# Optimization experiments

Measured on AMD Instinct MI355X. Metric: run time of the kernel, lower is better.

## Reference

```python
import jax, jax.numpy as jnp
import numpy as np

N_HEADS, N_LEVELS, N_POINTS = 8, 4, 4
D_MODEL, D_FFN = 256, 2048
NQ, BS = 900, 4
SPATIAL = np.array([[128, 128], [64, 64], [32, 32], [16, 16]], dtype=np.int64)
HW = int((SPATIAL[:, 0] * SPATIAL[:, 1]).sum())


def _ln(x, g, b):
    mu = x.mean(-1, keepdims=True)
    var = x.var(-1, keepdims=True)
    return (x - mu) / jnp.sqrt(var + 1e-5) * g + b


def _lin(x, w, b):
    return x @ w.T + b


def _msdeform_attn(query, refp, mem, ss, starts, so_w, so_b, aw_w, aw_b, vp_w, vp_b, op_w, op_b):
    # query: (bs, nq, d), refp: (bs, nq, L, 2) in [0,1], mem: (bs, hw, d)
    bs, nq, d = query.shape
    hd = d // N_HEADS
    value = _lin(mem, vp_w, vp_b).reshape(bs, -1, N_HEADS, hd)  # (bs, hw, H, hd)
    offsets = _lin(query, so_w, so_b).reshape(bs, nq, N_HEADS, N_LEVELS, N_POINTS, 2)
    aw = _lin(query, aw_w, aw_b).reshape(bs, nq, N_HEADS, N_LEVELS * N_POINTS)
    aw = jax.nn.softmax(aw, axis=-1).reshape(bs, nq, N_HEADS, N_LEVELS, N_POINTS)
    # offset normalizer is (W, H) per level
    normalizer = jnp.asarray(ss[:, ::-1].copy(), dtype=query.dtype)  # (L, 2)
    loc = refp[:, :, None, :, None, :] + offsets / normalizer[None, None, None, :, None, :]
    out = jnp.zeros((bs, nq, N_HEADS, hd), dtype=query.dtype)
    for l in range(N_LEVELS):
        h_l, w_l = int(ss[l, 0]), int(ss[l, 1])
        vl = value[:, starts[l]:starts[l] + h_l * w_l]  # (bs, h*w, H, hd)
        # grid_sample align_corners=False: pixel coord = loc*size - 0.5
        x = loc[:, :, :, l, :, 0] * w_l - 0.5  # (bs, nq, H, P)
        y = loc[:, :, :, l, :, 1] * h_l - 0.5
        x0 = jnp.floor(x)
        y0 = jnp.floor(y)
        fx = x - x0
        fy = y - y0

        def gather(ix, iy, wgt):
            valid = (ix >= 0) & (ix < w_l) & (iy >= 0) & (iy < h_l)
            idx = (jnp.clip(iy, 0, h_l - 1) * w_l + jnp.clip(ix, 0, w_l - 1)).astype(jnp.int32)
            # (bs, nq, H, P) -> (bs, nq*P, H) to match vl's (bs, hw, H, hd)
            idxt = idx.transpose(0, 1, 3, 2).reshape(bs, nq * N_POINTS, N_HEADS)
            g = jnp.take_along_axis(vl, idxt[..., None], axis=1)  # (bs, nq*P, H, hd)
            g = g.reshape(bs, nq, N_POINTS, N_HEADS, hd).transpose(0, 1, 3, 2, 4)
            return g * (wgt * valid)[..., None]

        x0i = x0.astype(jnp.int32)
        y0i = y0.astype(jnp.int32)
        sampled = (gather(x0i, y0i, (1 - fx) * (1 - fy))
                   + gather(x0i + 1, y0i, fx * (1 - fy))
                   + gather(x0i, y0i + 1, (1 - fx) * fy)
                   + gather(x0i + 1, y0i + 1, fx * fy))  # (bs, nq, H, P, hd)
        out = out + (sampled * aw[:, :, :, l, :, None]).sum(axis=3)
    return _lin(out.reshape(bs, nq, d), op_w, op_b)


def _fwd(tgt, query_pos, memory, ref_points,
         sa_in_w, sa_in_b, sa_out_w, sa_out_b,
         ln1_g, ln1_b, ln2_g, ln2_b, ln3_g, ln3_b,
         so_w, so_b, aw_w, aw_b, vp_w, vp_b, op_w, op_b,
         ff1_w, ff1_b, ff2_w, ff2_b, spatial_shapes, level_start_index):
    nq, bs, d = tgt.shape
    hd = d // N_HEADS
    ss = np.asarray(spatial_shapes)
    starts = np.asarray(level_start_index)
    # ---- self attention (q = k = tgt + pos, v = tgt) ----
    qk = tgt + query_pos
    q = _lin(qk, sa_in_w[:d], sa_in_b[:d]).reshape(nq, bs, N_HEADS, hd)
    k = _lin(qk, sa_in_w[d:2 * d], sa_in_b[d:2 * d]).reshape(nq, bs, N_HEADS, hd)
    v = _lin(tgt, sa_in_w[2 * d:], sa_in_b[2 * d:]).reshape(nq, bs, N_HEADS, hd)
    scores = jnp.einsum('qbhd,kbhd->bhqk', q, k) / np.sqrt(hd).astype(tgt.dtype)
    attn = jax.nn.softmax(scores, axis=-1)
    sa = jnp.einsum('bhqk,kbhd->qbhd', attn, v).reshape(nq, bs, d)
    sa = _lin(sa, sa_out_w, sa_out_b)
    tgt = _ln(tgt + sa, ln2_g, ln2_b)
    # ---- deformable cross attention ----
    ca = _msdeform_attn((tgt + query_pos).transpose(1, 0, 2),
                        ref_points.transpose(1, 0, 2, 3),
                        memory.transpose(1, 0, 2), ss, starts,
                        so_w, so_b, aw_w, aw_b, vp_w, vp_b, op_w, op_b)
    tgt = _ln(tgt + ca.transpose(1, 0, 2), ln1_g, ln1_b)
    # ---- FFN ----
    ff = _lin(jax.nn.relu(_lin(tgt, ff1_w, ff1_b)), ff2_w, ff2_b)
    return _ln(tgt + ff, ln3_g, ln3_b)


def setup_inputs() -> dict:
    key = jax.random.key(0)
    ks = iter(jax.random.split(key, 32))
    d, dffn = D_MODEL, D_FFN
    nofs = N_HEADS * N_LEVELS * N_POINTS
    w = lambda *s: jax.random.normal(next(ks), s, dtype=jnp.float32) * 0.02
    starts = np.concatenate([[0], np.cumsum(SPATIAL[:, 0] * SPATIAL[:, 1])[:-1]]).astype(np.int64)
    return {
        'tgt': jax.random.normal(next(ks), (NQ, BS, d), dtype=jnp.float32),
        'query_pos': jax.random.normal(next(ks), (NQ, BS, d), dtype=jnp.float32),
        'memory': jax.random.normal(next(ks), (HW, BS, d), dtype=jnp.float32),
        'ref_points': jax.random.uniform(next(ks), (NQ, BS, N_LEVELS, 2), dtype=jnp.float32),
        'sa_in_w': w(3 * d, d), 'sa_in_b': w(3 * d), 'sa_out_w': w(d, d), 'sa_out_b': w(d),
        'ln1_g': jnp.ones((d,)), 'ln1_b': jnp.zeros((d,)),
        'ln2_g': jnp.ones((d,)), 'ln2_b': jnp.zeros((d,)),
        'ln3_g': jnp.ones((d,)), 'ln3_b': jnp.zeros((d,)),
        'so_w': w(nofs * 2, d), 'so_b': jax.random.normal(next(ks), (nofs * 2,), dtype=jnp.float32) * 0.5,
        'aw_w': w(nofs, d), 'aw_b': w(nofs),
        'vp_w': w(d, d), 'vp_b': w(d), 'op_w': w(d, d), 'op_b': w(d),
        'ff1_w': w(dffn, d), 'ff1_b': w(dffn), 'ff2_w': w(d, dffn), 'ff2_b': w(d),
        'spatial_shapes': SPATIAL, 'level_start_index': starts,
    }


def reference(tgt, query_pos, memory, ref_points, sa_in_w, sa_in_b, sa_out_w, sa_out_b, ln1_g, ln1_b, ln2_g, ln2_b, ln3_g, ln3_b, so_w, so_b, aw_w, aw_b, vp_w, vp_b, op_w, op_b, ff1_w, ff1_b, ff2_w, ff2_b, spatial_shapes, level_start_index):
    return _fwd(tgt, query_pos, memory, ref_points, sa_in_w, sa_in_b, sa_out_w, sa_out_b,
                ln1_g, ln1_b, ln2_g, ln2_b, ln3_g, ln3_b, so_w, so_b, aw_w, aw_b,
                vp_w, vp_b, op_w, op_b, ff1_w, ff1_b, ff2_w, ff2_b,
                spatial_shapes, level_start_index)
```

## Files before the change

### kernel.cpp

```cpp
#include <hip/hip_runtime.h>
#include <hip/hip_bf16.h>

#define D_MODEL 256
#define N_HEADS 8
#define HD 32
#define NQ 900
#define BS 4
#define MROWS (NQ * BS)
#define HW_TOT 21760
#define VROWS (HW_TOT * BS)

typedef __attribute__((ext_vector_type(8))) short bf16x8;
typedef __attribute__((ext_vector_type(4))) float f32x4;

__device__ inline short f2b(float f) {
  union { __hip_bfloat16 h; short s; } u;
  u.h = __float2bfloat16(f);
  return u.s;
}
__device__ inline float bu2f(unsigned short u) {
  union { unsigned int i; float f; } c;
  c.i = ((unsigned int)u) << 16;
  return c.f;
}
__device__ inline bf16x8 bzero8() {
  bf16x8 v;
#pragma unroll
  for (int j = 0; j < 8; ++j) v[j] = 0;
  return v;
}
__device__ inline f32x4 fzero4() {
  f32x4 v;
#pragma unroll
  for (int j = 0; j < 4; ++j) v[j] = 0.f;
  return v;
}

#define GLL16(gsrc, ldst)                                                     \
  __builtin_amdgcn_global_load_lds(                                           \
      (__attribute__((address_space(1))) void*)(gsrc),                        \
      (__attribute__((address_space(3))) void*)(ldst), 16, 0, 0)

__global__ __launch_bounds__(256) void prep_all(const float* __restrict__ s0,
                                                const float* __restrict__ s1,
                                                const float* __restrict__ s2,
                                                const float* __restrict__ s3,
                                                const float* __restrict__ s4,
                                                const float* __restrict__ s5,
                                                const float* __restrict__ s6,
                                                const float* __restrict__ s7,
                                                short* __restrict__ dst,
                                                const float* __restrict__ tgt,
                                                const float* __restrict__ qpos,
                                                short* __restrict__ tgtb,
                                                short* __restrict__ qkb,
                                                const float* __restrict__ so_b,
                                                const float* __restrict__ aw_b,
                                                float* __restrict__ biasSOAW) {
  int i = blockIdx.x * 256 + threadIdx.x;
  if (i < 1540096) {
    const float* s; int off;
    if (i < 196608)      { s = s0; off = 0; }
    else if (i < 262144) { s = s1; off = 196608; }
    else if (i < 327680) { s = s2; off = 262144; }
    else if (i < 360448) { s = s3; off = 327680; }
    else if (i < 425984) { s = s4; off = 360448; }
    else if (i < 491520) { s = s5; off = 425984; }
    else if (i < 1015808){ s = s6; off = 491520; }
    else                 { s = s7; off = 1015808; }
    dst[i] = f2b(s[i - off]);
  } else {
    int j = i - 1540096;
    float t = tgt[j], p = qpos[j];
    tgtb[j] = f2b(t);
    qkb[j] = f2b(t + p);
    if (j < 384) biasSOAW[j] = (j < 256) ? so_b[j] : aw_b[j - 256];
  }
}

template <int BN, int AF32, int OUTF32, int RELU>
__device__ __forceinline__ void gemm_core(const void* __restrict__ Xv,
                                          const short* __restrict__ W,
                                          const float* __restrict__ bias,
                                          void* __restrict__ outv,
                                          int M, int N, int K, int m0, int n0,
                                          int t0, int t1, int addBias,
                                          short* __restrict__ smem) {
  constexpr int NF = BN / 16;
  short* sA = smem;
  short* sB = smem + 2 * 2048;
  const int tid = threadIdx.x;
  const int wave = tid >> 6, lane = tid & 63;
  const int l15 = lane & 15, l4 = lane >> 4;
  const int wr = wave * 16;
  const float* Xf = (const float*)Xv;
  const short* Xh = (const short*)Xv;

  f32x4 acc[NF];
#pragma unroll
  for (int f = 0; f < NF; ++f) acc[f] = fzero4();

  const int alr = wave * 16 + (lane >> 2);
  const int ags = (lane & 3) ^ ((alr >> 1) & 3);
  const int arow = tid >> 2, ak = tid & 3;
  const int agsrc = ak ^ ((arow >> 1) & 3);
  float4 ra0, ra1;

  auto stageB = [&](int t, int buf) {
    short* bb = sB + buf * BN * 32;
#pragma unroll
    for (int j = 0; j < BN / 64; ++j) {
      int lr = j * 64 + alr;
      int gs = (lane & 3) ^ ((lr >> 1) & 3);
      const short* src = W + (size_t)(n0 + lr) * K + t * 32 + gs * 8;
      GLL16(src, bb + (j * 64 + wave * 16) * 32);
    }
  };
  auto stageA_gll = [&](int t, int buf) {
    const short* src = Xh + (size_t)(m0 + alr) * K + t * 32 + ags * 8;
    GLL16(src, sA + buf * 2048 + wave * 512);
  };
  auto loadA_f32 = [&](int t) {
    const float* p = Xf + (size_t)(m0 + arow) * K + t * 32 + agsrc * 8;
    ra0 = *reinterpret_cast<const float4*>(p);
    ra1 = *reinterpret_cast<const float4*>(p + 4);
  };
  auto writeA_f32 = [&](int buf) {
    bf16x8 v;
    v[0] = f2b(ra0.x); v[1] = f2b(ra0.y); v[2] = f2b(ra0.z); v[3] = f2b(ra0.w);
    v[4] = f2b(ra1.x); v[5] = f2b(ra1.y); v[6] = f2b(ra1.z); v[7] = f2b(ra1.w);
    *reinterpret_cast<bf16x8*>(&sA[buf * 2048 + arow * 32 + ak * 8]) = v;
  };
  auto compute = [&](int buf) {
    const int r = wr + l15;
    bf16x8 av = *reinterpret_cast<const bf16x8*>(
        &sA[buf * 2048 + r * 32 + ((l4 ^ ((r >> 1) & 3)) * 8)]);
#pragma unroll
    for (int f = 0; f < NF; ++f) {
      const int rb = f * 16 + l15;
      bf16x8 bv = *reinterpret_cast<const bf16x8*>(
          &sB[buf * BN * 32 + rb * 32 + ((l4 ^ ((rb >> 1) & 3)) * 8)]);
      acc[f] = __builtin_amdgcn_mfma_f32_16x16x32_bf16(av, bv, acc[f], 0, 0, 0);
    }
  };

  if constexpr (AF32) { loadA_f32(t0); writeA_f32(0); }
  else stageA_gll(t0, 0);
  stageB(t0, 0);
  __syncthreads();

  int buf = 0;
  for (int t = t0; t < t1; ++t) {
    if (t + 1 < t1) {
      if constexpr (AF32) loadA_f32(t + 1);
      else stageA_gll(t + 1, buf ^ 1);
      stageB(t + 1, buf ^ 1);
    }
    compute(buf);
    if (AF32 && t + 1 < t1) writeA_f32(buf ^ 1);
    __syncthreads();
    buf ^= 1;
  }

#pragma unroll
  for (int f = 0; f < NF; ++f) {
    int col = n0 + f * 16 + l15;
    float bfv = addBias ? bias[col] : 0.f;
#pragma unroll
    for (int i = 0; i < 4; ++i) {
      int row = m0 + wr + l4 * 4 + i;
      if (row >= M) continue;
      float v = acc[f][i] + bfv;
      if (RELU) v = fmaxf(v, 0.f);
      if constexpr (OUTF32)
        ((float*)outv)[(size_t)row * N + col] = v;
      else
        ((short*)outv)[(size_t)row * N + col] = f2b(v);
    }
  }
}

template <int BN, int AF32, int OUTF32, int RELU>
__global__ __launch_bounds__(256) void gemm2(const void* __restrict__ Xv,
                                             const short* __restrict__ W,
                                             const float* __restrict__ bias,
                                             void* __restrict__ outv,
                                             int M, int N, int K) {
  __shared__ __align__(16) short smem[2 * 2048 + 2 * BN * 32];
  gemm_core<BN, AF32, OUTF32, RELU>(Xv, W, bias, outv, M, N, K,
                                    blockIdx.x * 64, blockIdx.y * BN,
                                    0, K / 32, 1, smem);
}

__global__ __launch_bounds__(256) void gemm_splitk(const void* __restrict__ Xv,
                                                   const short* __restrict__ W,
                                                   const float* __restrict__ bias,
                                                   float* __restrict__ outp,
                                                   int M, int N, int K) {
  __shared__ __align__(16) short smem[2 * 2048 + 2 * 64 * 32];
  const int kc = blockIdx.z;
  const int ntc = K / 32 / 2;
  gemm_core<64, 0, 1, 0>(Xv, W, bias, outp + (size_t)kc * M * N, M, N, K,
                         blockIdx.x * 64, blockIdx.y * 64,
                         kc * ntc, (kc + 1) * ntc, kc == 0, smem);
}

__global__ __launch_bounds__(256) void qkv_gemm(const short* __restrict__ qkb,
                                                const short* __restrict__ tgtb,
                                                const short* __restrict__ Wqkv,
                                                const float* __restrict__ sa_in_b,
                                                short* __restrict__ QKb,
                                                short* __restrict__ Vb) {
  __shared__ __align__(16) short smem[2 * 2048 + 2 * 64 * 32];
  int bx = blockIdx.x;
  if (bx < 456) {
    gemm_core<64, 0, 0, 0>(qkb, Wqkv, sa_in_b, QKb, MROWS, 512, 256,
                           (bx % 57) * 64, (bx / 57) * 64, 0, 8, 1, smem);
  } else {
    bx -= 456;
    gemm_core<64, 0, 0, 0>(tgtb, Wqkv + 512 * 256, sa_in_b + 512, Vb, MROWS, 256, 256,
                           (bx % 57) * 64, (bx / 57) * 64, 0, 8, 1, smem);
  }
}

__device__ __forceinline__ void flash_body(const short* __restrict__ QK,
                                           const short* __restrict__ V,
                                           short* __restrict__ O,
                                           int bid, short* __restrict__ smem) {
  const int bh = bid & 31, b = bh >> 3, h = bh & 7;
  const int q0 = (bid >> 5) * 64;
  const int tid = threadIdx.x, wave = tid >> 6, lane = tid & 63;
  const int l15 = lane & 15, l4 = lane >> 4;
  const int cb = h * 32;

  short* sQ = smem;
  short* sK = smem + 2048;
  short* sVt = smem + 6144;
  short* sP = smem + 10752;

  const int sr = wave * 16 + (lane >> 2);
  const int sgs = (lane & 3) ^ (sr & 3);

  auto stageK = [&](int kt, int buf) {
    const short* src = QK + (size_t)((kt * 64 + sr) * 4 + b) * 512 + 256 + cb + sgs * 8;
    GLL16(src, sK + buf * 2048 + wave * 512);
  };
  const int vrow = tid >> 2, vdof = (tid & 3) * 8;
  const int vkp = vrow ^ (((vdof >> 3) & 3) << 4);
  auto loadV = [&](int kt) -> bf16x8 {
    int kk = kt * 64 + vrow;
    return (kk < NQ)
        ? *reinterpret_cast<const bf16x8*>(V + (size_t)(kk * 4 + b) * 256 + cb + vdof)
        : bzero8();
  };
  auto writeV = [&](bf16x8 vv, int buf) {
    short* dst = sVt + buf * 2304;
#pragma unroll
    for (int j = 0; j < 8; ++j) dst[(vdof + j) * 72 + vkp] = vv[j];
  };

  {
    const short* qsrc = QK + (size_t)((q0 + sr) * 4 + b) * 512 + cb + sgs * 8;
    GLL16(qsrc, sQ + wave * 512);
  }
  stageK(0, 0);
  {
    bf16x8 v0 = loadV(0);
    writeV(v0, 0);
  }
  __syncthreads();

  const int wr = wave * 16;
  const int rq = wr + l15;
  const bf16x8 aq = *reinterpret_cast<const bf16x8*>(&sQ[rq * 32 + ((l4 ^ (rq & 3)) * 8)]);

  float mrow[4], lrow[4];
#pragma unroll
  for (int i = 0; i < 4; ++i) { mrow[i] = -1e30f; lrow[i] = 0.f; }
  f32x4 accO[2];
  accO[0] = fzero4(); accO[1] = fzero4();

  const int pswz = (((wr >> 2) + l4) & 3) << 3;
  const int pswzr = (((wr >> 2) + (l15 >> 2)) & 3) << 3;

  for (int kt = 0; kt < 15; ++kt) {
    const int k0 = kt * 64;
    const int buf = kt & 1;
    const bool more = (kt + 1 < 15);
    bf16x8 vnext = bzero8();
    if (more) {
      stageK(kt + 1, buf ^ 1);
      vnext = loadV(kt + 1);
    }

    f32x4 s[4];
#pragma unroll
    for (int f = 0; f < 4; ++f) {
      const int rb = f * 16 + l15;
      bf16x8 bk = *reinterpret_cast<bf16x8*>(
          &sK[buf * 2048 + rb * 32 + ((l4 ^ (rb & 3)) * 8)]);
      s[f] = __builtin_amdgcn_mfma_f32_16x16x32_bf16(aq, bk, fzero4(), 0, 0, 0);
    }
#pragma unroll
    for (int f = 0; f < 4; ++f) {
      bool valid = (k0 + f * 16 + l15) < NQ;
#pragma unroll
      for (int i = 0; i < 4; ++i) {
        float sv = s[f][i] * 0.17677669529663687f;
        s[f][i] = valid ? sv : -1e30f;
      }
    }
    float mx[4];
#pragma unroll
    for (int i = 0; i < 4; ++i)
      mx[i] = fmaxf(fmaxf(s[0][i], s[1][i]), fmaxf(s[2][i], s[3][i]));
#pragma unroll
    for (int off = 1; off < 16; off <<= 1)
#pragma unroll
      for (int i = 0; i < 4; ++i) mx[i] = fmaxf(mx[i], __shfl_xor(mx[i], off));

    float alpha[4], rs[4];
#pragma unroll
    for (int i = 0; i < 4; ++i) {
      float mn = fmaxf(mrow[i], mx[i]);
      alpha[i] = __expf(mrow[i] - mn);
      mrow[i] = mn;
      rs[i] = 0.f;
    }
#pragma unroll
    for (int f = 0; f < 4; ++f)
#pragma unroll
      for (int i = 0; i < 4; ++i) {
        float p = __expf(s[f][i] - mrow[i]);
        rs[i] += p;
        sP[(wr + l4 * 4 + i) * 72 + ((f * 16 + l15) ^ pswz)] = f2b(p);
      }
#pragma unroll
    for (int off = 1; off < 16; off <<= 1)
#pragma unroll
      for (int i = 0; i < 4; ++i) rs[i] += __shfl_xor(rs[i], off);
#pragma unroll
    for (int i = 0; i < 4; ++i) lrow[i] = lrow[i] * alpha[i] + rs[i];
#pragma unroll
    for (int nf = 0; nf < 2; ++nf)
#pragma unroll
      for (int i = 0; i < 4; ++i) accO[nf][i] *= alpha[i];

#pragma unroll
    for (int ks = 0; ks < 2; ++ks) {
      bf16x8 ap = *reinterpret_cast<bf16x8*>(
          &sP[(wr + l15) * 72 + ((ks * 32 + l4 * 8) ^ pswzr)]);
#pragma unroll
      for (int nf = 0; nf < 2; ++nf) {
        const int d = nf * 16 + l15;
        const int kb = (ks * 32 + l4 * 8) ^ (((d >> 3) & 3) << 4);
        bf16x8 bv = *reinterpret_cast<bf16x8*>(&sVt[buf * 2304 + d * 72 + kb]);
        accO[nf] = __builtin_amdgcn_mfma_f32_16x16x32_bf16(ap, bv, accO[nf], 0, 0, 0);
      }
    }
    if (more) writeV(vnext, buf ^ 1);
    __syncthreads();
  }

#pragma unroll
  for (int nf = 0; nf < 2; ++nf)
#pragma unroll
    for (int i = 0; i < 4; ++i) {
      int q = q0 + wr + l4 * 4 + i;
      if (q < NQ)
        O[(size_t)(q * 4 + b) * 256 + cb + nf * 16 + l15] = f2b(accO[nf][i] / lrow[i]);
    }
}

__device__ __forceinline__ void value_core(const float* __restrict__ memory,
                                           const short* __restrict__ W,
                                           const float* __restrict__ vp_b,
                                           short* __restrict__ value, int vb,
                                           short* __restrict__ smem) {
  float* sAf = (float*)smem;
  short* sB = smem + 8192;
  const int tid = threadIdx.x;
  const int wave = tid >> 6, lane = tid & 63;
  const int l15 = lane & 15, l4 = lane >> 4;
  const int wr = wave * 16;
  const int m0 = (((vb >> 4) << 3) | (vb & 7)) * 64;
  const int n0 = ((vb >> 3) & 1) * 128;

  const int ar0 = wave * 16 + (lane >> 3);
  const int ag = (lane & 7) ^ (lane >> 3);
  auto stageA = [&](int t, int buf) {
    const float* s0 = memory + (size_t)(m0 + ar0) * 256 + t * 32 + ag * 4;
    GLL16(s0, (short*)sAf + buf * 4096 + wave * 1024);
    const float* s1 = memory + (size_t)(m0 + ar0 + 8) * 256 + t * 32 + ag * 4;
    GLL16(s1, (short*)sAf + buf * 4096 + wave * 1024 + 512);
  };
  const int blr = wave * 16 + (lane >> 2);
  auto stageB = [&](int t, int buf) {
#pragma unroll
    for (int j = 0; j < 2; ++j) {
      int lr = j * 64 + blr;
      int gs = (lane & 3) ^ ((lr >> 1) & 3);
      const short* src = W + (size_t)(n0 + lr) * 256 + t * 32 + gs * 8;
      GLL16(src, sB + buf * 4096 + (j * 64 + wave * 16) * 32);
    }
  };

  f32x4 acc[8];
#pragma unroll
  for (int f = 0; f < 8; ++f) acc[f] = fzero4();

  auto compute = [&](int buf) {
    const int r = wr + l15;
    const int rx = r & 7;
    const float* ap = sAf + buf * 2048 + r * 32;
    float4 a0 = *reinterpret_cast<const float4*>(ap + (((2 * l4) ^ rx) * 4));
    float4 a1 = *reinterpret_cast<const float4*>(ap + (((2 * l4 + 1) ^ rx) * 4));
    bf16x8 av;
    av[0] = f2b(a0.x); av[1] = f2b(a0.y); av[2] = f2b(a0.z); av[3] = f2b(a0.w);
    av[4] = f2b(a1.x); av[5] = f2b(a1.y); av[6] = f2b(a1.z); av[7] = f2b(a1.w);
#pragma unroll
    for (int f = 0; f < 8; ++f) {
      const int rb = f * 16 + l15;
      bf16x8 bv = *reinterpret_cast<const bf16x8*>(
          &sB[buf * 4096 + rb * 32 + ((l4 ^ ((rb >> 1) & 3)) * 8)]);
      acc[f] = __builtin_amdgcn_mfma_f32_16x16x32_bf16(av, bv, acc[f], 0, 0, 0);
    }
  };

  stageA(0, 0); stageB(0, 0);
  stageA(1, 1); stageB(1, 1);
  asm volatile("s_waitcnt vmcnt(4)" ::: "memory");
  __builtin_amdgcn_sched_barrier(0);
  __builtin_amdgcn_s_barrier();
  __builtin_amdgcn_sched_barrier(0);

#pragma unroll
  for (int t = 0; t < 8; ++t) {
    const int buf = t & 1;
    compute(buf);
    asm volatile("s_waitcnt lgkmcnt(0)" ::: "memory");
    __builtin_amdgcn_sched_barrier(0);
    __builtin_amdgcn_s_barrier();
    __builtin_amdgcn_sched_barrier(0);
    if (t + 2 < 8) { stageA(t + 2, buf); stageB(t + 2, buf); }
    if (t + 1 < 8) {
      if (t + 2 < 8) asm volatile("s_waitcnt vmcnt(4)" ::: "memory");
      else           asm volatile("s_waitcnt vmcnt(0)" ::: "memory");
      __builtin_amdgcn_sched_barrier(0);
      __builtin_amdgcn_s_barrier();
      __builtin_amdgcn_sched_barrier(0);
    }
  }

#pragma unroll
  for (int f = 0; f < 8; ++f) {
    const int col = n0 + f * 16 + l15;
    const float bb = vp_b[col];
#pragma unroll
    for (int i = 0; i < 4; ++i)
      value[(size_t)(m0 + wr + l4 * 4 + i) * 256 + col] = f2b(acc[f][i] + bb);
  }
}

__global__ __launch_bounds__(256) void flash_value(const short* __restrict__ QKb,
                                                   const short* __restrict__ Vb,
                                                   short* __restrict__ Ob,
                                                   const float* __restrict__ memory,
                                                   const short* __restrict__ Wvp,
                                                   const float* __restrict__ vp_b,
                                                   short* __restrict__ value) {
  __shared__ __align__(16) short smem[16384];
  int bx = blockIdx.x;
  if (bx < 480) {
    flash_body(QKb, Vb, Ob, bx, smem);
  } else {
    value_core(memory, Wvp, vp_b, value, bx - 480, smem);
  }
}

__global__ __launch_bounds__(256) void ln_kernel(const float* __restrict__ A,
                                                 const float* __restrict__ B,
                                                 const float* __restrict__ g,
                                                 const float* __restrict__ bb,
                                                 float* __restrict__ outF,
                                                 short* __restrict__ outB,
                                                 const float* __restrict__ addv) {
  const int row = blockIdx.x;
  const int t = threadIdx.x;
  const size_t base = (size_t)row * D_MODEL;
  float x = A[base + t] + B[base + t];
  float s = x, s2 = x * x;
#pragma unroll
  for (int off = 32; off; off >>= 1) {
    s += __shfl_xor(s, off);
    s2 += __shfl_xor(s2, off);
  }
  __shared__ float wsum[4], wsum2[4];
  const int w = t >> 6;
  if ((t & 63) == 0) { wsum[w] = s; wsum2[w] = s2; }
  __syncthreads();
  s = wsum[0] + wsum[1] + wsum[2] + wsum[3];
  s2 = wsum2[0] + wsum2[1] + wsum2[2] + wsum2[3];
  const float mu = s * (1.f / 256.f);
  const float var = s2 * (1.f / 256.f) - mu * mu;
  const float inv = rsqrtf(var + 1e-5f);
  float y = (x - mu) * inv * g[t] + bb[t];
  outF[base + t] = y;
  if (outB) outB[base + t] = f2b(y + (addv ? addv[base + t] : 0.f));
}

__global__ __launch_bounds__(256) void ln4_kernel(const float* __restrict__ A,
                                                  const float* __restrict__ P,
                                                  const float* __restrict__ g,
                                                  const float* __restrict__ bb,
                                                  float* __restrict__ outF) {
  const int row = blockIdx.x;
  const int t = threadIdx.x;
  const size_t base = (size_t)row * D_MODEL + t;
  const size_t stride = (size_t)MROWS * D_MODEL;
  float x = A[base] + P[base] + P[base + stride];
  float s = x, s2 = x * x;
#pragma unroll
  for (int off = 32; off; off >>= 1) {
    s += __shfl_xor(s, off);
    s2 += __shfl_xor(s2, off);
  }
  __shared__ float wsum[4], wsum2[4];
  const int w = t >> 6;
  if ((t & 63) == 0) { wsum[w] = s; wsum2[w] = s2; }
  __syncthreads();
  s = wsum[0] + wsum[1] + wsum[2] + wsum[3];
  s2 = wsum2[0] + wsum2[1] + wsum2[2] + wsum2[3];
  const float mu = s * (1.f / 256.f);
  const float var = s2 * (1.f / 256.f) - mu * mu;
  const float inv = rsqrtf(var + 1e-5f);
  outF[base] = (x - mu) * inv * g[t] + bb[t];
}

__global__ __launch_bounds__(256) void msds_kernel(const unsigned short* __restrict__ value,
                                                   const float* __restrict__ soaw,
                                                   const float* __restrict__ refp,
                                                   unsigned short* __restrict__ out) {
  const int tid = threadIdx.x;
  const int row = blockIdx.x * 8 + (tid >> 5);
  const int lane32 = tid & 31;
  const int h = lane32 >> 2;
  const int dp = (lane32 & 3) * 8;
  const int b = row & 3;

  const int WL[4] = {128, 64, 32, 16};
  const int ST[4] = {0, 16384, 20480, 21504};

  const float* awp = soaw + (size_t)row * 384 + 256 + h * 16;
  float awv[16];
  float m = -1e30f;
#pragma unroll
  for (int i = 0; i < 16; ++i) { awv[i] = awp[i]; m = fmaxf(m, awv[i]); }
  float s = 0.f;
#pragma unroll
  for (int i = 0; i < 16; ++i) { awv[i] = __expf(awv[i] - m); s += awv[i]; }
  const float invs = 1.f / s;

  const float* offp = soaw + (size_t)row * 384 + h * 32;
  float acc[8];
#pragma unroll
  for (int j = 0; j < 8; ++j) acc[j] = 0.f;

#pragma unroll
  for (int l = 0; l < 4; ++l) {
    const int wl = WL[l], hl = WL[l], st = ST[l];
    const float rx = refp[((size_t)row * 4 + l) * 2 + 0];
    const float ry = refp[((size_t)row * 4 + l) * 2 + 1];
#pragma unroll
    for (int p = 0; p < 4; ++p) {
      const float ox = offp[l * 8 + p * 2 + 0];
      const float oy = offp[l * 8 + p * 2 + 1];
      const float x = (rx + ox / (float)wl) * (float)wl - 0.5f;
      const float y = (ry + oy / (float)hl) * (float)hl - 0.5f;
      const float x0f = floorf(x), y0f = floorf(y);
      const int x0 = (int)x0f, y0 = (int)y0f;
      const float fx = x - x0f, fy = y - y0f;
      const float a = awv[l * 4 + p] * invs;
      const float w00 = (1.f - fx) * (1.f - fy);
      const float w10 = fx * (1.f - fy);
      const float w01 = (1.f - fx) * fy;
      const float w11 = fx * fy;
      float sv[8];
#pragma unroll
      for (int j = 0; j < 8; ++j) sv[j] = 0.f;
      auto gat = [&](int ix, int iy, float wgt) {
        if (ix >= 0 && ix < wl && iy >= 0 && iy < hl) {
          const unsigned short* p2 =
              value + ((size_t)((st + iy * wl + ix) * 4 + b)) * 256 + h * 32 + dp;
          bf16x8 u = *reinterpret_cast<const bf16x8*>(p2);
#pragma unroll
          for (int j = 0; j < 8; ++j) sv[j] += wgt * bu2f((unsigned short)u[j]);
        }
      };
      gat(x0, y0, w00);
      gat(x0 + 1, y0, w10);
      gat(x0, y0 + 1, w01);
      gat(x0 + 1, y0 + 1, w11);
#pragma unroll
      for (int j = 0; j < 8; ++j) acc[j] += a * sv[j];
    }
  }
  bf16x8 o;
#pragma unroll
  for (int j = 0; j < 8; ++j) o[j] = f2b(acc[j]);
  *reinterpret_cast<bf16x8*>(&out[(size_t)row * 256 + h * 32 + dp]) = o;
}

extern "C" void kernel_launch(void* const* d_in, const int* in_sizes, int n_in,
                              void* d_out, int out_size, void* d_ws, size_t ws_size,
                              hipStream_t stream) {
  const float* tgt      = (const float*)d_in[0];
  const float* qpos     = (const float*)d_in[1];
  const float* memory   = (const float*)d_in[2];
  const float* refp     = (const float*)d_in[3];
  const float* sa_in_w  = (const float*)d_in[4];
  const float* sa_in_b  = (const float*)d_in[5];
  const float* sa_out_w = (const float*)d_in[6];
  const float* sa_out_b = (const float*)d_in[7];
  const float* ln1_g = (const float*)d_in[8];
  const float* ln1_b = (const float*)d_in[9];
  const float* ln2_g = (const float*)d_in[10];
  const float* ln2_b = (const float*)d_in[11];
  const float* ln3_g = (const float*)d_in[12];
  const float* ln3_b = (const float*)d_in[13];
  const float* so_w = (const float*)d_in[14];
  const float* so_b = (const float*)d_in[15];
  const float* aw_w = (const float*)d_in[16];
  const float* aw_b = (const float*)d_in[17];
  const float* vp_w = (const float*)d_in[18];
  const float* vp_b = (const float*)d_in[19];
  const float* op_w = (const float*)d_in[20];
  const float* op_b = (const float*)d_in[21];
  const float* ff1_w = (const float*)d_in[22];
  const float* ff1_b = (const float*)d_in[23];
  const float* ff2_w = (const float*)d_in[24];
  const float* ff2_b = (const float*)d_in[25];

  float* out = (float*)d_out;
  float* ws = (float*)d_ws;

  short* Wb       = (short*)ws;
  float* biasSOAW = ws + 770048;
  short* tgtb   = (short*)(ws + 770432);
  short* qkb    = (short*)(ws + 1231232);
  short* QKb    = (short*)(ws + 1692032);
  short* Vb     = (short*)(ws + 2613632);
  short* Ob     = (short*)(ws + 3074432);
  float* SA     = ws + 3535232;
  float* F      = ws + 4456832;
  short* qk2b   = (short*)(ws + 5378432);
  float* SOAW   = ws + 5839232;
  short* value  = (short*)(ws + 7221632);
  short* sampled= (short*)(ws + 18362752);
  float* CA     = ws + 18823552;
  float* tgt3   = ws + 19745152;
  short* tgt3b  = (short*)(ws + 20666752);
  short* H      = (short*)(ws + 21127552);
  float* FFp    = ws + 7221632;

  const short* Wqkv = Wb;
  const short* Wsa  = Wb + 196608;
  const short* Wso  = Wb + 262144;
  const short* Wvp  = Wb + 360448;
  const short* Wop  = Wb + 425984;
  const short* Wff1 = Wb + 491520;
  const short* Wff2 = Wb + 1015808;

  prep_all<<<9616, 256, 0, stream>>>(sa_in_w, sa_out_w, so_w, aw_w, vp_w, op_w,
                                     ff1_w, ff2_w, Wb, tgt, qpos, tgtb, qkb,
                                     so_b, aw_b, biasSOAW);
  qkv_gemm<<<684, 256, 0, stream>>>(qkb, tgtb, Wqkv, sa_in_b, QKb, Vb);
  flash_value<<<3200, 256, 0, stream>>>(QKb, Vb, Ob, memory, Wvp, vp_b, value);
  gemm2<64, 0, 1, 0><<<dim3(57, 4), 256, 0, stream>>>(Ob, Wsa, sa_out_b, SA, MROWS, 256, 256);
  ln_kernel<<<MROWS, 256, 0, stream>>>(tgt, SA, ln2_g, ln2_b, F, qk2b, qpos);
  gemm2<64, 0, 1, 0><<<dim3(57, 6), 256, 0, stream>>>(qk2b, Wso, biasSOAW, SOAW, MROWS, 384, 256);
  msds_kernel<<<450, 256, 0, stream>>>((const unsigned short*)value, SOAW, refp,
                                       (unsigned short*)sampled);
  gemm2<64, 0, 1, 0><<<dim3(57, 4), 256, 0, stream>>>(sampled, Wop, op_b, CA, MROWS, 256, 256);
  ln_kernel<<<MROWS, 256, 0, stream>>>(F, CA, ln1_g, ln1_b, tgt3, tgt3b, nullptr);
  gemm2<64, 0, 0, 1><<<dim3(57, 32), 256, 0, stream>>>(tgt3b, Wff1, ff1_b, H, MROWS, 2048, 256);
  gemm_splitk<<<dim3(57, 4, 2), 256, 0, stream>>>(H, Wff2, ff2_b, FFp, MROWS, 256, 2048);
  ln4_kernel<<<MROWS, 256, 0, stream>>>(tgt3, FFp, ln3_g, ln3_b, out);
}
```

Baseline: 161.2 us.

## Split flash attention over key halves and split-K the small GEMMs

Self-attention blocks now each process half of the key tiles and write unnormalized partial outputs plus running max and sum. A new merge kernel combines the two halves into the bf16 attention output. The three 256-wide GEMMs (sa_out, sampling-offset/attention-weight, output projection) now use split-K with two partial buffers, which the LayerNorm kernels and the sampling kernel sum on read. The aim is more blocks for an under-filled GPU, at the cost of an extra launch, extra fp32 partial traffic and a reshuffled workspace.

Measured after the change: 170.1 us. 1.06x slower.

```diff
diff --git a/kernel.cpp b/kernel.cpp
--- a/kernel.cpp
+++ b/kernel.cpp
@@ -9,6 +9,7 @@
 #define MROWS (NQ * BS)
 #define HW_TOT 21760
 #define VROWS (HW_TOT * BS)
+#define PSTRIDE (MROWS * D_MODEL)
 
 typedef __attribute__((ext_vector_type(8))) short bf16x8;
 typedef __attribute__((ext_vector_type(4))) float f32x4;
@@ -93,7 +94,6 @@
   const int wave = tid >> 6, lane = tid & 63;
   const int l15 = lane & 15, l4 = lane >> 4;
   const int wr = wave * 16;
-  const float* Xf = (const float*)Xv;
   const short* Xh = (const short*)Xv;
 
   f32x4 acc[NF];
@@ -102,9 +102,6 @@
 
   const int alr = wave * 16 + (lane >> 2);
   const int ags = (lane & 3) ^ ((alr >> 1) & 3);
-  const int arow = tid >> 2, ak = tid & 3;
-  const int agsrc = ak ^ ((arow >> 1) & 3);
-  float4 ra0, ra1;
 
   auto stageB = [&](int t, int buf) {
     short* bb = sB + buf * BN * 32;
@@ -120,17 +117,6 @@
     const short* src = Xh + (size_t)(m0 + alr) * K + t * 32 + ags * 8;
     GLL16(src, sA + buf * 2048 + wave * 512);
   };
-  auto loadA_f32 = [&](int t) {
-    const float* p = Xf + (size_t)(m0 + arow) * K + t * 32 + agsrc * 8;
-    ra0 = *reinterpret_cast<const float4*>(p);
-    ra1 = *reinterpret_cast<const float4*>(p + 4);
-  };
-  auto writeA_f32 = [&](int buf) {
-    bf16x8 v;
-    v[0] = f2b(ra0.x); v[1] = f2b(ra0.y); v[2] = f2b(ra0.z); v[3] = f2b(ra0.w);
-    v[4] = f2b(ra1.x); v[5] = f2b(ra1.y); v[6] = f2b(ra1.z); v[7] = f2b(ra1.w);
-    *reinterpret_cast<bf16x8*>(&sA[buf * 2048 + arow * 32 + ak * 8]) = v;
-  };
   auto compute = [&](int buf) {
     const int r = wr + l15;
     bf16x8 av = *reinterpret_cast<const bf16x8*>(
@@ -144,20 +130,17 @@
     }
   };
 
-  if constexpr (AF32) { loadA_f32(t0); writeA_f32(0); }
-  else stageA_gll(t0, 0);
+  stageA_gll(t0, 0);
   stageB(t0, 0);
   __syncthreads();
 
   int buf = 0;
   for (int t = t0; t < t1; ++t) {
     if (t + 1 < t1) {
-      if constexpr (AF32) loadA_f32(t + 1);
-      else stageA_gll(t + 1, buf ^ 1);
+      stageA_gll(t + 1, buf ^ 1);
       stageB(t + 1, buf ^ 1);
     }
     compute(buf);
-    if (AF32 && t + 1 < t1) writeA_f32(buf ^ 1);
     __syncthreads();
     buf ^= 1;
   }
@@ -225,10 +208,14 @@
 
 __device__ __forceinline__ void flash_body(const short* __restrict__ QK,
                                            const short* __restrict__ V,
-                                           short* __restrict__ O,
+                                           float* __restrict__ Opart,
+                                           float* __restrict__ ML,
                                            int bid, short* __restrict__ smem) {
   const int bh = bid & 31, b = bh >> 3, h = bh & 7;
-  const int q0 = (bid >> 5) * 64;
+  const int rest = bid >> 5;
+  const int q0 = (rest >> 1) * 64;
+  const int kh = rest & 1;
+  const int kt0 = kh * 8, kt1 = kh ? 15 : 8;
   const int tid = threadIdx.x, wave = tid >> 6, lane = tid & 63;
   const int l15 = lane & 15, l4 = lane >> 4;
   const int cb = h * 32;
@@ -263,9 +250,9 @@
     const short* qsrc = QK + (size_t)((q0 + sr) * 4 + b) * 512 + cb + sgs * 8;
     GLL16(qsrc, sQ + wave * 512);
   }
-  stageK(0, 0);
+  stageK(kt0, 0);
   {
-    bf16x8 v0 = loadV(0);
+    bf16x8 v0 = loadV(kt0);
     writeV(v0, 0);
   }
   __syncthreads();
@@ -283,10 +270,10 @@
   const int pswz = (((wr >> 2) + l4) & 3) << 3;
   const int pswzr = (((wr >> 2) + (l15 >> 2)) & 3) << 3;
 
-  for (int kt = 0; kt < 15; ++kt) {
+  for (int kt = kt0; kt < kt1; ++kt) {
     const int k0 = kt * 64;
-    const int buf = kt & 1;
-    const bool more = (kt + 1 < 15);
+    const int buf = (kt - kt0) & 1;
+    const bool more = (kt + 1 < kt1);
     bf16x8 vnext = bzero8();
     if (more) {
       stageK(kt + 1, buf ^ 1);
@@ -368,8 +355,38 @@
     for (int i = 0; i < 4; ++i) {
       int q = q0 + wr + l4 * 4 + i;
       if (q < NQ)
-        O[(size_t)(q * 4 + b) * 256 + cb + nf * 16 + l15] = f2b(accO[nf][i] / lrow[i]);
-    }
+        Opart[(size_t)kh * PSTRIDE + (size_t)(q * 4 + b) * 256 + cb + nf * 16 + l15] =
+            accO[nf][i];
+    }
+  if (l15 == 0) {
+#pragma unroll
+    for (int i = 0; i < 4; ++i) {
+      int q = q0 + wr + l4 * 4 + i;
+      if (q < NQ) {
+        const size_t mi = ((size_t)kh * MROWS + (q * 4 + b)) * 8 + h;
+        ML[mi * 2 + 0] = mrow[i];
+        ML[mi * 2 + 1] = lrow[i];
+      }
+    }
+  }
+}
+
+__global__ __launch_bounds__(256) void flash_merge(const float* __restrict__ Opart,
+                                                   const float* __restrict__ ML,
+                                                   short* __restrict__ Ob) {
+  const int row = blockIdx.x;
+  const int col = threadIdx.x;
+  const int h = col >> 5;
+  const size_t m1i = ((size_t)row) * 8 + h;
+  const size_t m2i = ((size_t)MROWS + row) * 8 + h;
+  const float m1 = ML[m1i * 2 + 0], l1 = ML[m1i * 2 + 1];
+  const float m2 = ML[m2i * 2 + 0], l2 = ML[m2i * 2 + 1];
+  const float M = fmaxf(m1, m2);
+  const float a1 = __expf(m1 - M), a2 = __expf(m2 - M);
+  const float denom = a1 * l1 + a2 * l2;
+  const size_t idx = (size_t)row * 256 + col;
+  const float o = (a1 * Opart[idx] + a2 * Opart[PSTRIDE + idx]) / denom;
+  Ob[idx] = f2b(o);
 }
 
 __device__ __forceinline__ void value_core(const float* __restrict__ memory,
@@ -464,31 +481,32 @@
 
 __global__ __launch_bounds__(256) void flash_value(const short* __restrict__ QKb,
                                                    const short* __restrict__ Vb,
-                                                   short* __restrict__ Ob,
+                                                   float* __restrict__ Opart,
+                                                   float* __restrict__ ML,
                                                    const float* __restrict__ memory,
                                                    const short* __restrict__ Wvp,
                                                    const float* __restrict__ vp_b,
                                                    short* __restrict__ value) {
   __shared__ __align__(16) short smem[16384];
   int bx = blockIdx.x;
-  if (bx < 480) {
-    flash_body(QKb, Vb, Ob, bx, smem);
+  if (bx < 960) {
+    flash_body(QKb, Vb, Opart, ML, bx, smem);
   } else {
-    value_core(memory, Wvp, vp_b, value, bx - 480, smem);
-  }
-}
-
-__global__ __launch_bounds__(256) void ln_kernel(const float* __restrict__ A,
-                                                 const float* __restrict__ B,
-                                                 const float* __restrict__ g,
-                                                 const float* __restrict__ bb,
-                                                 float* __restrict__ outF,
-                                                 short* __restrict__ outB,
-                                                 const float* __restrict__ addv) {
+    value_core(memory, Wvp, vp_b, value, bx - 960, smem);
+  }
+}
+
+__global__ __launch_bounds__(256) void lnp_kernel(const float* __restrict__ A,
+                                                  const float* __restrict__ P,
+                                                  const float* __restrict__ g,
+                                                  const float* __restrict__ bb,
+                                                  float* __restrict__ outF,
+                                                  short* __restrict__ outB,
+                                                  const float* __restrict__ addv) {
   const int row = blockIdx.x;
   const int t = threadIdx.x;
-  const size_t base = (size_t)row * D_MODEL;
-  float x = A[base + t] + B[base + t];
+  const size_t base = (size_t)row * D_MODEL + t;
+  float x = A[base] + P[base] + P[base + PSTRIDE];
   float s = x, s2 = x * x;
 #pragma unroll
   for (int off = 32; off; off >>= 1) {
@@ -505,40 +523,12 @@
   const float var = s2 * (1.f / 256.f) - mu * mu;
   const float inv = rsqrtf(var + 1e-5f);
   float y = (x - mu) * inv * g[t] + bb[t];
-  outF[base + t] = y;
-  if (outB) outB[base + t] = f2b(y + (addv ? addv[base + t] : 0.f));
-}
-
-__global__ __launch_bounds__(256) void ln4_kernel(const float* __restrict__ A,
-                                                  const float* __restrict__ P,
-                                                  const float* __restrict__ g,
-                                                  const float* __restrict__ bb,
-                                                  float* __restrict__ outF) {
-  const int row = blockIdx.x;
-  const int t = threadIdx.x;
-  const size_t base = (size_t)row * D_MODEL + t;
-  const size_t stride = (size_t)MROWS * D_MODEL;
-  float x = A[base] + P[base] + P[base + stride];
-  float s = x, s2 = x * x;
-#pragma unroll
-  for (int off = 32; off; off >>= 1) {
-    s += __shfl_xor(s, off);
-    s2 += __shfl_xor(s2, off);
-  }
-  __shared__ float wsum[4], wsum2[4];
-  const int w = t >> 6;
-  if ((t & 63) == 0) { wsum[w] = s; wsum2[w] = s2; }
-  __syncthreads();
-  s = wsum[0] + wsum[1] + wsum[2] + wsum[3];
-  s2 = wsum2[0] + wsum2[1] + wsum2[2] + wsum2[3];
-  const float mu = s * (1.f / 256.f);
-  const float var = s2 * (1.f / 256.f) - mu * mu;
-  const float inv = rsqrtf(var + 1e-5f);
-  outF[base] = (x - mu) * inv * g[t] + bb[t];
+  outF[base] = y;
+  if (outB) outB[base] = f2b(y + (addv ? addv[base] : 0.f));
 }
 
 __global__ __launch_bounds__(256) void msds_kernel(const unsigned short* __restrict__ value,
-                                                   const float* __restrict__ soaw,
+                                                   const float* __restrict__ soawp,
                                                    const float* __restrict__ refp,
                                                    unsigned short* __restrict__ out) {
   const int tid = threadIdx.x;
@@ -547,21 +537,25 @@
   const int h = lane32 >> 2;
   const int dp = (lane32 & 3) * 8;
   const int b = row & 3;
+  const int SOSTRIDE = MROWS * 384;
 
   const int WL[4] = {128, 64, 32, 16};
   const int ST[4] = {0, 16384, 20480, 21504};
 
-  const float* awp = soaw + (size_t)row * 384 + 256 + h * 16;
+  const float* awp = soawp + (size_t)row * 384 + 256 + h * 16;
   float awv[16];
   float m = -1e30f;
 #pragma unroll
-  for (int i = 0; i < 16; ++i) { awv[i] = awp[i]; m = fmaxf(m, awv[i]); }
+  for (int i = 0; i < 16; ++i) {
+    awv[i] = awp[i] + awp[SOSTRIDE + i];
+    m = fmaxf(m, awv[i]);
+  }
   float s = 0.f;
 #pragma unroll
   for (int i = 0; i < 16; ++i) { awv[i] = __expf(awv[i] - m); s += awv[i]; }
   const float invs = 1.f / s;
 
-  const float* offp = soaw + (size_t)row * 384 + h * 32;
+  const float* offp = soawp + (size_t)row * 384 + h * 32;
   float acc[8];
 #pragma unroll
   for (int j = 0; j < 8; ++j) acc[j] = 0.f;
@@ -573,8 +567,8 @@
     const float ry = refp[((size_t)row * 4 + l) * 2 + 1];
 #pragma unroll
     for (int p = 0; p < 4; ++p) {
-      const float ox = offp[l * 8 + p * 2 + 0];
-      const float oy = offp[l * 8 + p * 2 + 1];
+      const float ox = offp[l * 8 + p * 2 + 0] + offp[SOSTRIDE + l * 8 + p * 2 + 0];
+      const float oy = offp[l * 8 + p * 2 + 1] + offp[SOSTRIDE + l * 8 + p * 2 + 1];
       const float x = (rx + ox / (float)wl) * (float)wl - 0.5f;
       const float y = (ry + oy / (float)hl) * (float)hl - 0.5f;
       const float x0f = floorf(x), y0f = floorf(y);
@@ -647,21 +641,23 @@
   short* Wb       = (short*)ws;
   float* biasSOAW = ws + 770048;
   short* tgtb   = (short*)(ws + 770432);
-  short* qkb    = (short*)(ws + 1231232);
-  short* QKb    = (short*)(ws + 1692032);
-  short* Vb     = (short*)(ws + 2613632);
-  short* Ob     = (short*)(ws + 3074432);
-  float* SA     = ws + 3535232;
-  float* F      = ws + 4456832;
-  short* qk2b   = (short*)(ws + 5378432);
-  float* SOAW   = ws + 5839232;
-  short* value  = (short*)(ws + 7221632);
-  short* sampled= (short*)(ws + 18362752);
-  float* CA     = ws + 18823552;
-  float* tgt3   = ws + 19745152;
-  short* tgt3b  = (short*)(ws + 20666752);
-  short* H      = (short*)(ws + 21127552);
-  float* FFp    = ws + 7221632;
+  short* qkb    = (short*)(ws + 1000832);
+  short* QKb    = (short*)(ws + 1231232);
+  short* Vb     = (short*)(ws + 1692032);
+  short* Ob     = (short*)(ws + 1922432);
+  float* F      = ws + 2152832;
+  short* qk2b   = (short*)(ws + 3074432);
+  float* SAp    = ws + 3304832;
+  float* tgt3   = ws + 5148032;
+  short* tgt3b  = (short*)(ws + 6069632);
+  short* sampled= (short*)(ws + 6300032);
+  float* Opart  = ws + 6530432;
+  float* CAp    = ws + 6530432;
+  float* FFp    = ws + 6530432;
+  float* ML     = ws + 8373632;
+  short* value  = (short*)(ws + 8488832);
+  float* SOAWp  = ws + 19629952;
+  short* H      = (short*)(ws + 22394752);
 
   const short* Wqkv = Wb;
   const short* Wsa  = Wb + 196608;
@@ -675,15 +671,16 @@
                                      ff1_w, ff2_w, Wb, tgt, qpos, tgtb, qkb,
                                      so_b, aw_b, biasSOAW);
   qkv_gemm<<<684, 256, 0, stream>>>(qkb, tgtb, Wqkv, sa_in_b, QKb, Vb);
-  flash_value<<<3200, 256, 0, stream>>>(QKb, Vb, Ob, memory, Wvp, vp_b, value);
-  gemm2<64, 0, 1, 0><<<dim3(57, 4), 256, 0, stream>>>(Ob, Wsa, sa_out_b, SA, MROWS, 256, 256);
-  ln_kernel<<<MROWS, 256, 0, stream>>>(tgt, SA, ln2_g, ln2_b, F, qk2b, qpos);
-  gemm2<64, 0, 1, 0><<<dim3(57, 6), 256, 0, stream>>>(qk2b, Wso, biasSOAW, SOAW, MROWS, 384, 256);
-  msds_kernel<<<450, 256, 0, stream>>>((const unsigned short*)value, SOAW, refp,
+  flash_value<<<3680, 256, 0, stream>>>(QKb, Vb, Opart, ML, memory, Wvp, vp_b, value);
+  flash_merge<<<MROWS, 256, 0, stream>>>(Opart, ML, Ob);
+  gemm_splitk<<<dim3(57, 4, 2), 256, 0, stream>>>(Ob, Wsa, sa_out_b, SAp, MROWS, 256, 256);
+  lnp_kernel<<<MROWS, 256, 0, stream>>>(tgt, SAp, ln2_g, ln2_b, F, qk2b, qpos);
+  gemm_splitk<<<dim3(57, 6, 2), 256, 0, stream>>>(qk2b, Wso, biasSOAW, SOAWp, MROWS, 384, 256);
+  msds_kernel<<<450, 256, 0, stream>>>((const unsigned short*)value, SOAWp, refp,
                                        (unsigned short*)sampled);
-  gemm2<64, 0, 1, 0><<<dim3(57, 4), 256, 0, stream>>>(sampled, Wop, op_b, CA, MROWS, 256, 256);
-  ln_kernel<<<MROWS, 256, 0, stream>>>(F, CA, ln1_g, ln1_b, tgt3, tgt3b, nullptr);
+  gemm_splitk<<<dim3(57, 4, 2), 256, 0, stream>>>(sampled, Wop, op_b, CAp, MROWS, 256, 256);
+  lnp_kernel<<<MROWS, 256, 0, stream>>>(F, CAp, ln1_g, ln1_b, tgt3, tgt3b, nullptr);
   gemm2<64, 0, 0, 1><<<dim3(57, 32), 256, 0, stream>>>(tgt3b, Wff1, ff1_b, H, MROWS, 2048, 256);
   gemm_splitk<<<dim3(57, 4, 2), 256, 0, stream>>>(H, Wff2, ff2_b, FFp, MROWS, 256, 2048);
-  ln4_kernel<<<MROWS, 256, 0, stream>>>(tgt3, FFp, ln3_g, ln3_b, out);
-}
+  lnp_kernel<<<MROWS, 256, 0, stream>>>(tgt3, FFp, ln3_g, ln3_b, out, nullptr, nullptr);
+}
```
